# Performance work log

Measured on AMD Instinct MI355X. Metric: run time of the kernel, lower is better.

The kernel has to match this reference:

```python
import jax, jax.numpy as jnp
import numpy as np

HID = 1024   # hidden_dim
H = 16       # num_head
D = 64       # head_dim
W = 64       # window_size (one-sided attention radius)


def setup_inputs() -> dict:
    key = jax.random.key(0)
    ks = jax.random.split(key, 10)
    B, S = 2, 4096
    s = 0.02
    X = jax.random.normal(ks[0], (B, S, HID), jnp.float32)
    mask = jnp.ones((B, S), jnp.float32)
    Wq = jax.random.normal(ks[1], (HID, H * D), jnp.float32) * s
    bq = jnp.zeros((H * D,), jnp.float32)
    Wk = jax.random.normal(ks[2], (HID, H * D), jnp.float32) * s
    bk = jnp.zeros((H * D,), jnp.float32)
    Wv = jax.random.normal(ks[3], (HID, H * D), jnp.float32) * s
    bv = jnp.zeros((H * D,), jnp.float32)
    Wo = jax.random.normal(ks[4], (H * D, HID), jnp.float32) * s
    bo = jnp.zeros((HID,), jnp.float32)
    return dict(X=X, mask=mask, Wq=Wq, bq=bq, Wk=Wk, bk=bk, Wv=Wv, bv=bv, Wo=Wo, bo=bo)


def _chunk3(T, nC):
    # T: [B,H,S,D] -> [B,H,nC,3W,D]: for chunk c, keys of chunks c-1, c, c+1 (zero-padded at ends)
    B, Hh, S, Dd = T.shape
    Tp = jnp.pad(T, ((0, 0), (0, 0), (W, W), (0, 0))).reshape(B, Hh, nC + 2, W, Dd)
    return jnp.concatenate([Tp[:, :, :-2], Tp[:, :, 1:-1], Tp[:, :, 2:]], axis=3)


def reference(X, mask, Wq, bq, Wk, bk, Wv, bv, Wo, bo):
    B, S0, _ = X.shape
    pad = W - S0 % W  # matches torch: always >= 1 (full window if divisible)
    Xp = jnp.pad(X, ((0, 0), (0, pad), (0, 0)))
    mp = jnp.pad(mask, ((0, 0), (0, pad)))  # padded keys masked out
    S = S0 + pad
    nC = S // W

    def proj(Wm, b):
        return (Xp @ Wm + b).reshape(B, S, H, D).transpose(0, 2, 1, 3)  # [B,H,S,D]

    Q, K, V = proj(Wq, bq), proj(Wk, bk), proj(Wv, bv)
    Qc = Q.reshape(B, H, nC, W, D)
    K3 = _chunk3(K, nC)
    V3 = _chunk3(V, nC)

    # banded scores: query i attends keys j with |i - j| <= W
    scores = jnp.einsum('bhcqd,bhckd->bhcqk', Qc, K3) / jnp.asarray(np.sqrt(D), jnp.float32)
    qi = jnp.arange(W)[:, None]
    kj = jnp.arange(3 * W)[None, :]
    band = (kj >= qi) & (kj <= qi + 2 * W)  # [W, 3W]
    m3 = jnp.pad(mp, ((0, 0), (W, W))).reshape(B, nC + 2, W)
    m3 = jnp.concatenate([m3[:, :-2], m3[:, 1:-1], m3[:, 2:]], axis=2)  # [B,nC,3W]
    valid = band[None, None, None, :, :] & (m3[:, None, :, None, :] > 0)
    scores = jnp.where(valid, scores, -1e9)
    A = jax.nn.softmax(scores, axis=-1)
    ctx = jnp.einsum('bhcqk,bhckd->bhcqd', A, V3).reshape(B, H, S, D)
    out = ctx.transpose(0, 2, 1, 3).reshape(B, S, H * D) @ Wo + bo
    return out[:, :S0]
```

## Files before the change

### kernel.cpp

```cpp
#include <hip/hip_runtime.h>

typedef unsigned short u16;
typedef unsigned int u32;
typedef __bf16 bf16x8 __attribute__((ext_vector_type(8)));
typedef u16 u16x8 __attribute__((ext_vector_type(8)));
typedef float floatx4 __attribute__((ext_vector_type(4)));

#define MFMA16(a, b, c) __builtin_amdgcn_mfma_f32_16x16x32_bf16((a), (b), (c), 0, 0, 0)

#define B_ 2
#define S0 4096
#define NH 16
#define HD 64
#define HID 1024

__device__ __forceinline__ float bf2f(u16 u) {
  union { u32 i; float f; } x; x.i = ((u32)u) << 16; return x.f;
}
__device__ __forceinline__ u16 f2bf(float f) {
  union { float f; u32 i; } x; x.f = f;
  u32 r = x.i + 0x7FFFu + ((x.i >> 16) & 1u);
  return (u16)(r >> 16);
}

__device__ __forceinline__ void glds16(const u16* g, u16* l) {
  __builtin_amdgcn_global_load_lds(
      (const __attribute__((address_space(1))) u32*)g,
      (__attribute__((address_space(3))) u32*)l, 16, 0, 0);
}

__global__ __launch_bounds__(256) void convert_x(const float* __restrict__ X,
                                                 u16* __restrict__ dst) {
  int i = (blockIdx.x * 256 + threadIdx.x) * 8;
  u16x8 v;
#pragma unroll
  for (int j = 0; j < 8; j++) v[j] = f2bf(X[i + j]);
  *(u16x8*)(dst + i) = v;
}

__global__ __launch_bounds__(256) void convert_small(
    const float* __restrict__ mask, const float* __restrict__ bq,
    const float* __restrict__ bk, const float* __restrict__ bv,
    const float* __restrict__ bo, u16* __restrict__ cmask,
    u16* __restrict__ cb) {
  int tid = blockIdx.x * 256 + threadIdx.x;
  if (tid < B_ * S0) {
    cmask[tid] = f2bf(mask[tid]);
  } else {
    int j = tid - B_ * S0;
    int seg = j >> 10, idx = j & 1023;
    const float* src = (seg == 0) ? bq : (seg == 1) ? bk : (seg == 2) ? bv : bo;
    cb[seg * 1024 + idx] = f2bf(src[idx]);
  }
}

__global__ __launch_bounds__(256) void transpose4(
    const float* __restrict__ Wq, const float* __restrict__ Wk,
    const float* __restrict__ Wv, const float* __restrict__ Wo,
    u16* __restrict__ WqkvT, u16* __restrict__ WoT) {
  __shared__ u16 tile[64][66];
  int mat = blockIdx.z;
  const float* src = (mat == 0) ? Wq : (mat == 1) ? Wk : (mat == 2) ? Wv : Wo;
  u16* dst = (mat < 3) ? (WqkvT + (size_t)mat * HID * HID) : WoT;
  int t0 = blockIdx.x * 64;
  int c0 = blockIdx.y * 64;
  int tx = threadIdx.x & 63, ty = threadIdx.x >> 6;
#pragma unroll
  for (int i = 0; i < 16; i++) {
    int r = i * 4 + ty;
    tile[r][tx] = f2bf(src[(size_t)(t0 + r) * HID + c0 + tx]);
  }
  __syncthreads();
#pragma unroll
  for (int i = 0; i < 16; i++) {
    int r = i * 4 + ty;
    dst[(size_t)(c0 + r) * HID + t0 + tx] = tile[tx][r];
  }
}

__global__ __launch_bounds__(256) void gemm_bf16_tn(
    const u16* __restrict__ A, const u16* __restrict__ Bt,
    const u16* __restrict__ cb, void* __restrict__ outp, int K, int mode) {
  __shared__ alignas(16) u16 sA[128 * 32];
  __shared__ alignas(16) u16 sB[128 * 32];
  int t = threadIdx.x;
  int wave = t >> 6, lane = t & 63;
  int wm = wave >> 1, wn = wave & 1;
  int quad = lane >> 4, l16 = lane & 15;
  int tile_m = blockIdx.x * 128;
  int tile_n = blockIdx.y * 128;

  floatx4 acc[4][4] = {};

  int srow = wave * 16 + (lane >> 2);
  int scol = (lane & 3) * 8;
  const u16* Ag = A + (size_t)(tile_m + srow) * K + scol;
  const u16* Bg = Bt + (size_t)(tile_n + srow) * K + scol;
  u16* lA0 = sA + wave * 512;
  u16* lA1 = sA + 2048 + wave * 512;
  u16* lB0 = sB + wave * 512;
  u16* lB1 = sB + 2048 + wave * 512;
  size_t half = (size_t)64 * K;

  for (int k0 = 0; k0 < K; k0 += 32) {
    __syncthreads();
    glds16(Ag + k0, lA0);
    glds16(Ag + half + k0, lA1);
    glds16(Bg + k0, lB0);
    glds16(Bg + half + k0, lB1);
    __syncthreads();

    bf16x8 af[4], bfr[4];
#pragma unroll
    for (int mt = 0; mt < 4; mt++)
      af[mt] = *(const bf16x8*)(sA + (wm * 64 + mt * 16 + l16) * 32 + quad * 8);
#pragma unroll
    for (int nt = 0; nt < 4; nt++)
      bfr[nt] = *(const bf16x8*)(sB + (wn * 64 + nt * 16 + l16) * 32 + quad * 8);
#pragma unroll
    for (int mt = 0; mt < 4; mt++)
#pragma unroll
      for (int nt = 0; nt < 4; nt++)
        acc[mt][nt] = MFMA16(af[mt], bfr[nt], acc[mt][nt]);
  }

  if (mode == 0) {
    u16* op = (u16*)outp;
#pragma unroll
    for (int mt = 0; mt < 4; mt++) {
      int row0 = tile_m + wm * 64 + mt * 16 + quad * 4;
      int bb = row0 >> 12;
      int sbase = row0 & (S0 - 1);
#pragma unroll
      for (int nt = 0; nt < 4; nt++) {
        int col = tile_n + wn * 64 + nt * 16 + l16;
        int p = col >> 10;
        int rem = col & 1023;
        float bias = bf2f(cb[p * 1024 + rem]);
        int hh = rem >> 6, dd = rem & 63;
        u16* dp = op + ((size_t)(((p * 2 + bb) * NH + hh)) * S0 + sbase) * HD + dd;
#pragma unroll
        for (int r = 0; r < 4; r++)
          dp[(size_t)r * HD] = f2bf(acc[mt][nt][r] + bias);
      }
    }
  } else {
    float* op = (float*)outp;
#pragma unroll
    for (int mt = 0; mt < 4; mt++) {
      int row0 = tile_m + wm * 64 + mt * 16 + quad * 4;
#pragma unroll
      for (int nt = 0; nt < 4; nt++) {
        int col = tile_n + wn * 64 + nt * 16 + l16;
        float bias = bf2f(cb[3 * 1024 + col]);
        float* dp = op + (size_t)row0 * HID + col;
#pragma unroll
        for (int r = 0; r < 4; r++)
          dp[(size_t)r * HID] = acc[mt][nt][r] + bias;
      }
    }
  }
}

__global__ __launch_bounds__(256) void attn_win(
    const u16* __restrict__ Q, const u16* __restrict__ Kp,
    const u16* __restrict__ Vp, const u16* __restrict__ cmask,
    u16* __restrict__ ctx) {
  __shared__ alignas(16) u16 sVt[64 * 208];
  __shared__ alignas(16) u16 sP[4 * 16 * 200];
  __shared__ u16 sMk[208];

  int bid = blockIdx.x;
  int c = bid & 63;
  int h = (bid >> 6) & 15;
  int b = bid >> 10;
  int t = threadIdx.x;
  int wave = t >> 6, lane = t & 63;
  int quad = lane >> 4, l16 = lane & 15;
  int koff = wave * 16;

  const u16* Qb = Q + (size_t)(b * NH + h) * S0 * HD;
  const u16* Kb = Kp + (size_t)(b * NH + h) * S0 * HD;
  const u16* Vb = Vp + (size_t)(b * NH + h) * S0 * HD;
  int kbase = (c - 1) * 64;

#pragma unroll
  for (int i = 0; i < 7; i++) {
    int e = i * 256 + t;
    if (e < 1664) {
      int slot = e >> 3, d0 = (e & 7) * 8;
      int key = kbase + slot;
      int kc = key < 0 ? 0 : (key > S0 - 1 ? S0 - 1 : key);
      u16x8 v = *(const u16x8*)(Vb + (size_t)kc * HD + d0);
#pragma unroll
      for (int j = 0; j < 8; j++) sVt[(d0 + j) * 208 + slot] = v[j];
    }
  }
  if (t < 208) {
    int j = kbase + t;
    sMk[t] = (j >= 0 && j < S0) ? cmask[(size_t)b * S0 + j] : (u16)0;
  }
  __syncthreads();

  floatx4 sc[10] = {};
  int qrow = c * 64 + wave * 16 + l16;
#pragma unroll
  for (int ks = 0; ks < 2; ks++) {
    bf16x8 aq = *(const bf16x8*)(Qb + (size_t)qrow * HD + ks * 32 + quad * 8);
#pragma unroll
    for (int nt = 0; nt < 10; nt++) {
      int key = kbase + koff + nt * 16 + l16;
      int kc = key < 0 ? 0 : (key > S0 - 1 ? S0 - 1 : key);
      bf16x8 bk = *(const bf16x8*)(Kb + (size_t)kc * HD + ks * 32 + quad * 8);
      sc[nt] = MFMA16(aq, bk, sc[nt]);
    }
  }

  int qrel_base = wave * 16 + quad * 4;
  u16* myP = sP + wave * 16 * 200;
  float kmask[10];
#pragma unroll
  for (int nt = 0; nt < 10; nt++) kmask[nt] = bf2f(sMk[koff + nt * 16 + l16]);

#pragma unroll
  for (int reg = 0; reg < 4; reg++) {
    int qrel = qrel_base + reg;
    float v[10];
    float m = -3e38f;
#pragma unroll
    for (int nt = 0; nt < 10; nt++) {
      int jr = koff + nt * 16 + l16 - 64;
      bool ok = (jr >= qrel - 64) && (jr <= qrel + 64) && (kmask[nt] > 0.f);
      float s = ok ? sc[nt][reg] * 0.125f : -1e30f;
      v[nt] = s;
      m = fmaxf(m, s);
    }
#pragma unroll
    for (int off = 1; off <= 8; off <<= 1) m = fmaxf(m, __shfl_xor(m, off));
    float sum = 0.f;
#pragma unroll
    for (int nt = 0; nt < 10; nt++) {
      float p = __expf(v[nt] - m);
      v[nt] = p;
      sum += p;
    }
#pragma unroll
    for (int off = 1; off <= 8; off <<= 1) sum += __shfl_xor(sum, off);
    float inv = 1.0f / sum;
#pragma unroll
    for (int nt = 0; nt < 10; nt++)
      myP[(quad * 4 + reg) * 200 + nt * 16 + l16] = f2bf(v[nt] * inv);
  }
  __syncthreads();

  floatx4 oc[4] = {};
#pragma unroll
  for (int ks = 0; ks < 5; ks++) {
    bf16x8 ap = *(const bf16x8*)(myP + l16 * 200 + ks * 32 + quad * 8);
#pragma unroll
    for (int nt = 0; nt < 4; nt++) {
      bf16x8 bv =
          *(const bf16x8*)(sVt + (nt * 16 + l16) * 208 + koff + ks * 32 + quad * 8);
      oc[nt] = MFMA16(ap, bv, oc[nt]);
    }
  }

  int srow = c * 64 + wave * 16 + quad * 4;
#pragma unroll
  for (int nt = 0; nt < 4; nt++) {
    u16* dp = ctx + (size_t)(b * S0 + srow) * HID + h * HD + nt * 16 + l16;
#pragma unroll
    for (int reg = 0; reg < 4; reg++)
      dp[(size_t)reg * HID] = f2bf(oc[nt][reg]);
  }
}

extern "C" void kernel_launch(void* const* d_in, const int* in_sizes, int n_in,
                              void* d_out, int out_size, void* d_ws, size_t ws_size,
                              hipStream_t stream) {
  const float* X = (const float*)d_in[0];
  const float* mask = (const float*)d_in[1];
  const float* Wq = (const float*)d_in[2];
  const float* bq = (const float*)d_in[3];
  const float* Wk = (const float*)d_in[4];
  const float* bk = (const float*)d_in[5];
  const float* Wv = (const float*)d_in[6];
  const float* bv = (const float*)d_in[7];
  const float* Wo = (const float*)d_in[8];
  const float* bo = (const float*)d_in[9];
  char* ws = (char*)d_ws;

  const size_t MB = 1048576;
  u16* cmask = (u16*)(ws + 256);
  u16* cb = (u16*)(ws + 256 + 16384);
  u16* cX = (u16*)(ws + 1 * MB);
  u16* WqkvT = (u16*)(ws + 17 * MB);
  u16* WoT = (u16*)(ws + 23 * MB);
  u16* QKV = (u16*)(ws + 25 * MB);
  u16* CTX = cX;

  const size_t per_qkv = (size_t)B_ * NH * S0 * HD;

  convert_x<<<4096, 256, 0, stream>>>(X, cX);
  convert_small<<<48, 256, 0, stream>>>(mask, bq, bk, bv, bo, cmask, cb);
  transpose4<<<dim3(16, 16, 4), 256, 0, stream>>>(Wq, Wk, Wv, Wo, WqkvT, WoT);
  gemm_bf16_tn<<<dim3(64, 24), 256, 0, stream>>>(cX, WqkvT, cb, QKV, HID, 0);
  attn_win<<<dim3(B_ * NH * 64), 256, 0, stream>>>(QKV, QKV + per_qkv,
                                                   QKV + 2 * per_qkv, cmask, CTX);
  gemm_bf16_tn<<<dim3(64, 8), 256, 0, stream>>>(CTX, WoT, cb, d_out, HID, 1);
}
```

Before: 261.2 us.

## Merge prep kernels, deepen GEMM K-tile with XOR-swizzled LDS, fix V transpose mapping

Merges the three preprocessing kernels (X conversion, mask/bias conversion, weight transpose) into one launch to cut launch overhead. The GEMM K-step grows from 32 to 64 and uses an XOR-swizzled LDS layout, which halves the number of barrier pairs and avoids LDS bank conflicts on fragment reads. The attention V-transpose load is remapped so consecutive threads write consecutive key slots in LDS, reducing write bank conflicts at the cost of less coalesced global reads. LDS per GEMM block doubles, which may lower occupancy.

After: 234.8 us. 1.11x faster.

```diff
diff --git a/kernel.cpp b/kernel.cpp
--- a/kernel.cpp
+++ b/kernel.cpp
@@ -29,60 +29,59 @@
       (__attribute__((address_space(3))) u32*)l, 16, 0, 0);
 }
 
-__global__ __launch_bounds__(256) void convert_x(const float* __restrict__ X,
-                                                 u16* __restrict__ dst) {
-  int i = (blockIdx.x * 256 + threadIdx.x) * 8;
-  u16x8 v;
-#pragma unroll
-  for (int j = 0; j < 8; j++) v[j] = f2bf(X[i + j]);
-  *(u16x8*)(dst + i) = v;
-}
-
-__global__ __launch_bounds__(256) void convert_small(
-    const float* __restrict__ mask, const float* __restrict__ bq,
-    const float* __restrict__ bk, const float* __restrict__ bv,
-    const float* __restrict__ bo, u16* __restrict__ cmask,
-    u16* __restrict__ cb) {
-  int tid = blockIdx.x * 256 + threadIdx.x;
-  if (tid < B_ * S0) {
-    cmask[tid] = f2bf(mask[tid]);
-  } else {
-    int j = tid - B_ * S0;
-    int seg = j >> 10, idx = j & 1023;
-    const float* src = (seg == 0) ? bq : (seg == 1) ? bk : (seg == 2) ? bv : bo;
-    cb[seg * 1024 + idx] = f2bf(src[idx]);
-  }
-}
-
-__global__ __launch_bounds__(256) void transpose4(
-    const float* __restrict__ Wq, const float* __restrict__ Wk,
-    const float* __restrict__ Wv, const float* __restrict__ Wo,
+__global__ __launch_bounds__(256) void prep(
+    const float* __restrict__ X, const float* __restrict__ mask,
+    const float* __restrict__ Wq, const float* __restrict__ bq,
+    const float* __restrict__ Wk, const float* __restrict__ bk,
+    const float* __restrict__ Wv, const float* __restrict__ bv,
+    const float* __restrict__ Wo, const float* __restrict__ bo,
+    u16* __restrict__ cX, u16* __restrict__ cmask, u16* __restrict__ cb,
     u16* __restrict__ WqkvT, u16* __restrict__ WoT) {
   __shared__ u16 tile[64][66];
-  int mat = blockIdx.z;
-  const float* src = (mat == 0) ? Wq : (mat == 1) ? Wk : (mat == 2) ? Wv : Wo;
-  u16* dst = (mat < 3) ? (WqkvT + (size_t)mat * HID * HID) : WoT;
-  int t0 = blockIdx.x * 64;
-  int c0 = blockIdx.y * 64;
-  int tx = threadIdx.x & 63, ty = threadIdx.x >> 6;
-#pragma unroll
-  for (int i = 0; i < 16; i++) {
-    int r = i * 4 + ty;
-    tile[r][tx] = f2bf(src[(size_t)(t0 + r) * HID + c0 + tx]);
-  }
-  __syncthreads();
-#pragma unroll
-  for (int i = 0; i < 16; i++) {
-    int r = i * 4 + ty;
-    dst[(size_t)(c0 + r) * HID + t0 + tx] = tile[tx][r];
+  int bid = blockIdx.x;
+  if (bid < 4096) {
+    int i = (bid * 256 + threadIdx.x) * 8;
+    u16x8 v;
+#pragma unroll
+    for (int j = 0; j < 8; j++) v[j] = f2bf(X[i + j]);
+    *(u16x8*)(cX + i) = v;
+  } else if (bid < 4144) {
+    int tid = (bid - 4096) * 256 + threadIdx.x;
+    if (tid < B_ * S0) {
+      cmask[tid] = f2bf(mask[tid]);
+    } else {
+      int j = tid - B_ * S0;
+      int seg = j >> 10, idx = j & 1023;
+      const float* src = (seg == 0) ? bq : (seg == 1) ? bk : (seg == 2) ? bv : bo;
+      cb[seg * 1024 + idx] = f2bf(src[idx]);
+    }
+  } else {
+    int idx = bid - 4144;
+    int mat = idx >> 8;
+    const float* src = (mat == 0) ? Wq : (mat == 1) ? Wk : (mat == 2) ? Wv : Wo;
+    u16* dst = (mat < 3) ? (WqkvT + (size_t)mat * HID * HID) : WoT;
+    int t0 = ((idx >> 4) & 15) * 64;
+    int c0 = (idx & 15) * 64;
+    int tx = threadIdx.x & 63, ty = threadIdx.x >> 6;
+#pragma unroll
+    for (int i = 0; i < 16; i++) {
+      int r = i * 4 + ty;
+      tile[r][tx] = f2bf(src[(size_t)(t0 + r) * HID + c0 + tx]);
+    }
+    __syncthreads();
+#pragma unroll
+    for (int i = 0; i < 16; i++) {
+      int r = i * 4 + ty;
+      dst[(size_t)(c0 + r) * HID + t0 + tx] = tile[tx][r];
+    }
   }
 }
 
 __global__ __launch_bounds__(256) void gemm_bf16_tn(
     const u16* __restrict__ A, const u16* __restrict__ Bt,
     const u16* __restrict__ cb, void* __restrict__ outp, int K, int mode) {
-  __shared__ alignas(16) u16 sA[128 * 32];
-  __shared__ alignas(16) u16 sB[128 * 32];
+  __shared__ alignas(16) u16 sA[128 * 64];
+  __shared__ alignas(16) u16 sB[128 * 64];
   int t = threadIdx.x;
   int wave = t >> 6, lane = t & 63;
   int wm = wave >> 1, wn = wave & 1;
@@ -92,36 +91,43 @@
 
   floatx4 acc[4][4] = {};
 
-  int srow = wave * 16 + (lane >> 2);
-  int scol = (lane & 3) * 8;
-  const u16* Ag = A + (size_t)(tile_m + srow) * K + scol;
-  const u16* Bg = Bt + (size_t)(tile_n + srow) * K + scol;
-  u16* lA0 = sA + wave * 512;
-  u16* lA1 = sA + 2048 + wave * 512;
-  u16* lB0 = sB + wave * 512;
-  u16* lB1 = sB + 2048 + wave * 512;
-  size_t half = (size_t)64 * K;
-
-  for (int k0 = 0; k0 < K; k0 += 32) {
+  int row_l = lane >> 3;
+  int col_l = ((lane & 7) ^ row_l) * 8;
+  const u16* Ag = A + (size_t)(tile_m + wave * 8 + row_l) * K + col_l;
+  const u16* Bg = Bt + (size_t)(tile_n + wave * 8 + row_l) * K + col_l;
+  u16* lA = sA + wave * 8 * 64;
+  u16* lB = sB + wave * 8 * 64;
+
+  for (int k0 = 0; k0 < K; k0 += 64) {
     __syncthreads();
-    glds16(Ag + k0, lA0);
-    glds16(Ag + half + k0, lA1);
-    glds16(Bg + k0, lB0);
-    glds16(Bg + half + k0, lB1);
+#pragma unroll
+    for (int r = 0; r < 4; r++) {
+      glds16(Ag + (size_t)(r * 32) * K + k0, lA + r * 2048);
+      glds16(Bg + (size_t)(r * 32) * K + k0, lB + r * 2048);
+    }
     __syncthreads();
 
-    bf16x8 af[4], bfr[4];
-#pragma unroll
-    for (int mt = 0; mt < 4; mt++)
-      af[mt] = *(const bf16x8*)(sA + (wm * 64 + mt * 16 + l16) * 32 + quad * 8);
-#pragma unroll
-    for (int nt = 0; nt < 4; nt++)
-      bfr[nt] = *(const bf16x8*)(sB + (wn * 64 + nt * 16 + l16) * 32 + quad * 8);
-#pragma unroll
-    for (int mt = 0; mt < 4; mt++)
-#pragma unroll
-      for (int nt = 0; nt < 4; nt++)
-        acc[mt][nt] = MFMA16(af[mt], bfr[nt], acc[mt][nt]);
+#pragma unroll
+    for (int ks = 0; ks < 2; ks++) {
+      bf16x8 af[4], bfr[4];
+#pragma unroll
+      for (int mt = 0; mt < 4; mt++) {
+        int row = wm * 64 + mt * 16 + l16;
+        int p = (ks * 4 + quad) ^ (row & 7);
+        af[mt] = *(const bf16x8*)(sA + row * 64 + p * 8);
+      }
+#pragma unroll
+      for (int nt = 0; nt < 4; nt++) {
+        int row = wn * 64 + nt * 16 + l16;
+        int p = (ks * 4 + quad) ^ (row & 7);
+        bfr[nt] = *(const bf16x8*)(sB + row * 64 + p * 8);
+      }
+#pragma unroll
+      for (int mt = 0; mt < 4; mt++)
+#pragma unroll
+        for (int nt = 0; nt < 4; nt++)
+          acc[mt][nt] = MFMA16(af[mt], bfr[nt], acc[mt][nt]);
+    }
   }
 
   if (mode == 0) {
@@ -188,12 +194,13 @@
   for (int i = 0; i < 7; i++) {
     int e = i * 256 + t;
     if (e < 1664) {
-      int slot = e >> 3, d0 = (e & 7) * 8;
+      int dg = e / 208;
+      int slot = e - dg * 208;
       int key = kbase + slot;
       int kc = key < 0 ? 0 : (key > S0 - 1 ? S0 - 1 : key);
-      u16x8 v = *(const u16x8*)(Vb + (size_t)kc * HD + d0);
-#pragma unroll
-      for (int j = 0; j < 8; j++) sVt[(d0 + j) * 208 + slot] = v[j];
+      u16x8 v = *(const u16x8*)(Vb + (size_t)kc * HD + dg * 8);
+#pragma unroll
+      for (int j = 0; j < 8; j++) sVt[(dg * 8 + j) * 208 + slot] = v[j];
     }
   }
   if (t < 208) {
@@ -301,9 +308,8 @@
 
   const size_t per_qkv = (size_t)B_ * NH * S0 * HD;
 
-  convert_x<<<4096, 256, 0, stream>>>(X, cX);
-  convert_small<<<48, 256, 0, stream>>>(mask, bq, bk, bv, bo, cmask, cb);
-  transpose4<<<dim3(16, 16, 4), 256, 0, stream>>>(Wq, Wk, Wv, Wo, WqkvT, WoT);
+  prep<<<4096 + 48 + 1024, 256, 0, stream>>>(X, mask, Wq, bq, Wk, bk, Wv, bv,
+                                             Wo, bo, cX, cmask, cb, WqkvT, WoT);
   gemm_bf16_tn<<<dim3(64, 24), 256, 0, stream>>>(cX, WqkvT, cb, QKV, HID, 0);
   attn_win<<<dim3(B_ * NH * 64), 256, 0, stream>>>(QKV, QKV + per_qkv,
                                                    QKV + 2 * per_qkv, cmask, CTX);
```
